# Performance work log

Measured on AMD Instinct MI355X. Metric: run time of the kernel, lower is better.

Reference implementation:

```python
import jax, jax.numpy as jnp
import numpy as np

H = 128  # hidden_size

def _lstm_layer(x, w_ih, w_hh, b_ih, b_hh):
    # x: [B, T, D]; w_ih: [4H, D]; w_hh: [4H, H]; biases: [4H]
    B, T, _ = x.shape
    # Precompute input contributions for all timesteps (the big GEMM).
    xg = jnp.einsum('btd,gd->btg', x, w_ih) + b_ih + b_hh  # [B, T, 4H]
    xg = jnp.transpose(xg, (1, 0, 2))  # [T, B, 4H]
    w_hh_t = w_hh.T  # [H, 4H]

    def step(carry, xt):
        h, c = carry
        g = xt + h @ w_hh_t  # [B, 4H]
        i, f, gg, o = jnp.split(g, 4, axis=-1)  # PyTorch gate order i,f,g,o
        i = jax.nn.sigmoid(i)
        f = jax.nn.sigmoid(f)
        gg = jnp.tanh(gg)
        o = jax.nn.sigmoid(o)
        c = f * c + i * gg
        h = o * jnp.tanh(c)
        return (h, c), h

    h0 = jnp.zeros((B, H), dtype=x.dtype)
    c0 = jnp.zeros((B, H), dtype=x.dtype)
    _, hs = jax.lax.scan(step, (h0, c0), xg)  # hs: [T, B, H]
    return jnp.transpose(hs, (1, 0, 2))  # [B, T, H]

def setup_inputs() -> dict:
    key = jax.random.key(0)
    ks = jax.random.split(key, 11)
    s = 1.0 / np.sqrt(H)  # PyTorch LSTM init scale
    return {
        'x': jax.random.normal(ks[0], (128, 512, 1024), dtype=jnp.float32),
        'w_ih0': jax.random.normal(ks[1], (4 * H, 1024), dtype=jnp.float32) * s,
        'w_hh0': jax.random.normal(ks[2], (4 * H, H), dtype=jnp.float32) * s,
        'b_ih0': jax.random.normal(ks[3], (4 * H,), dtype=jnp.float32) * s,
        'b_hh0': jax.random.normal(ks[4], (4 * H,), dtype=jnp.float32) * s,
        'w_ih1': jax.random.normal(ks[5], (4 * H, H), dtype=jnp.float32) * s,
        'w_hh1': jax.random.normal(ks[6], (4 * H, H), dtype=jnp.float32) * s,
        'b_ih1': jax.random.normal(ks[7], (4 * H,), dtype=jnp.float32) * s,
        'b_hh1': jax.random.normal(ks[8], (4 * H,), dtype=jnp.float32) * s,
        'fc_w': jax.random.normal(ks[9], (8, H), dtype=jnp.float32) * s,
        'fc_b': jax.random.normal(ks[10], (8,), dtype=jnp.float32) * s,
    }

def reference(x, w_ih0, w_hh0, b_ih0, b_hh0, w_ih1, w_hh1, b_ih1, b_hh1, fc_w, fc_b):
    h1 = _lstm_layer(x, w_ih0, w_hh0, b_ih0, b_hh0)   # [B, T, H]
    h2 = _lstm_layer(h1, w_ih1, w_hh1, b_ih1, b_hh1)  # [B, T, H]
    logits = h2[:, -1, :] @ fc_w.T + fc_b             # [B, num_classes]
    return logits
```

## Files before the change

kernel.cpp:

```cpp
#include <hip/hip_runtime.h>
#include <hip/hip_bf16.h>

#define BATCH 128
#define TSTEPS 512
#define HID 128
#define GATES 512
#define M_TOTAL (BATCH * TSTEPS)

typedef _Float16 h2_t __attribute__((ext_vector_type(2)));

__device__ __forceinline__ float sigmoidf_fast(float x) {
    return 1.0f / (1.0f + __expf(-x));
}
__device__ __forceinline__ float tanhf_fast(float x) {
    return 1.0f - 2.0f / (__expf(2.0f * x) + 1.0f);
}

__device__ __forceinline__ float fdot2h(h2_t a, h2_t b, float c) {
#if __has_builtin(__builtin_amdgcn_fdot2)
    return __builtin_amdgcn_fdot2(a, b, c, false);
#else
    return c + (float)a[0] * (float)b[0] + (float)a[1] * (float)b[1];
#endif
}

template<int K>
__global__ __launch_bounds__(256) void gemm_bias_k(
    const float* __restrict__ A,
    const float* __restrict__ W,
    const float* __restrict__ b0,
    const float* __restrict__ b1,
    float* __restrict__ xgT)
{
    constexpr int BM = 128, BN = 128, BK = 16;
    __shared__ float As[BK][BM];
    __shared__ float Bs[BK][BN];

    const int tid = threadIdx.x;
    const int tx = tid & 15;
    const int ty = tid >> 4;
    const int n0 = blockIdx.x * BN;
    const int m0 = blockIdx.y * BM;

    const int f0 = tid, f1 = tid + 256;
    const int ar0 = f0 >> 2, ak0 = (f0 & 3) * 4;
    const int ar1 = f1 >> 2, ak1 = (f1 & 3) * 4;

    const float* pa0 = A + (size_t)(m0 + ar0) * K + ak0;
    const float* pa1 = A + (size_t)(m0 + ar1) * K + ak1;
    const float* pw0 = W + (size_t)(n0 + ar0) * K + ak0;
    const float* pw1 = W + (size_t)(n0 + ar1) * K + ak1;

    float bias8[8];
    #pragma unroll
    for (int j = 0; j < 8; ++j) {
        int n = n0 + ((j < 4) ? (tx * 4 + j) : (64 + tx * 4 + j - 4));
        bias8[j] = b0[n] + b1[n];
    }
    float acc[8][8];
    #pragma unroll
    for (int i = 0; i < 8; ++i)
        #pragma unroll
        for (int j = 0; j < 8; ++j) acc[i][j] = bias8[j];

    for (int k0 = 0; k0 < K; k0 += BK) {
        const float4 a0 = *(const float4*)(pa0 + k0);
        const float4 a1 = *(const float4*)(pa1 + k0);
        const float4 w0 = *(const float4*)(pw0 + k0);
        const float4 w1 = *(const float4*)(pw1 + k0);
        __syncthreads();
        As[ak0 + 0][ar0] = a0.x; As[ak0 + 1][ar0] = a0.y;
        As[ak0 + 2][ar0] = a0.z; As[ak0 + 3][ar0] = a0.w;
        As[ak1 + 0][ar1] = a1.x; As[ak1 + 1][ar1] = a1.y;
        As[ak1 + 2][ar1] = a1.z; As[ak1 + 3][ar1] = a1.w;
        Bs[ak0 + 0][ar0] = w0.x; Bs[ak0 + 1][ar0] = w0.y;
        Bs[ak0 + 2][ar0] = w0.z; Bs[ak0 + 3][ar0] = w0.w;
        Bs[ak1 + 0][ar1] = w1.x; Bs[ak1 + 1][ar1] = w1.y;
        Bs[ak1 + 2][ar1] = w1.z; Bs[ak1 + 3][ar1] = w1.w;
        __syncthreads();
        #pragma unroll
        for (int kk = 0; kk < BK; ++kk) {
            const float4 av0 = *(const float4*)&As[kk][ty * 8];
            const float4 av1 = *(const float4*)&As[kk][ty * 8 + 4];
            const float4 bv0 = *(const float4*)&Bs[kk][tx * 4];
            const float4 bv1 = *(const float4*)&Bs[kk][64 + tx * 4];
            const float a[8]  = {av0.x, av0.y, av0.z, av0.w, av1.x, av1.y, av1.z, av1.w};
            const float bb[8] = {bv0.x, bv0.y, bv0.z, bv0.w, bv1.x, bv1.y, bv1.z, bv1.w};
            #pragma unroll
            for (int i = 0; i < 8; ++i)
                #pragma unroll
                for (int j = 0; j < 8; ++j)
                    acc[i][j] = __fmaf_rn(a[i], bb[j], acc[i][j]);
        }
    }

    const int bi = m0 >> 9;
    const int t0 = (m0 & 511) + ty * 8;
    float4* xo = (float4*)xgT;
    #pragma unroll
    for (int j = 0; j < 8; ++j) {
        const int n = n0 + ((j < 4) ? (tx * 4 + j) : (64 + tx * 4 + j - 4));
        float4 v0 = make_float4(acc[0][j], acc[1][j], acc[2][j], acc[3][j]);
        float4 v1 = make_float4(acc[4][j], acc[5][j], acc[6][j], acc[7][j]);
        xo[(size_t)(bi * 128 + (t0 >> 2)) * 512 + n]     = v0;
        xo[(size_t)(bi * 128 + (t0 >> 2) + 1) * 512 + n] = v1;
    }
}

__global__ __launch_bounds__(1024, 4) void fused_rec(
    const float* __restrict__ xgT,
    const float* __restrict__ w_hh0,
    const float* __restrict__ w_ih1,
    const float* __restrict__ w_hh1,
    const float* __restrict__ b_ih1,
    const float* __restrict__ b_hh1,
    const float* __restrict__ fc_w,
    const float* __restrict__ fc_b,
    unsigned int* __restrict__ h1g,
    int* __restrict__ flags,
    float* __restrict__ logits)
{
    const int blk = blockIdx.x;
    const int L1  = blk >= BATCH;
    const int b   = blk & (BATCH - 1);
    const int tid = threadIdx.x;
    const int g   = tid >> 1;
    const int kh  = tid & 1;

    __shared__ h2_t h2s[64];
    __shared__ float act_s[GATES];
    __shared__ h2_t hin2[8 * 64];

    h2_t whh[32], wih[32];
    {
        const float* wr = (L1 ? w_hh1 : w_hh0) + (size_t)g * HID + kh * 64;
        #pragma unroll
        for (int i = 0; i < 32; ++i)
            whh[i] = (h2_t){(_Float16)wr[2 * i], (_Float16)wr[2 * i + 1]};
    }
    float bias = 0.f;
    if (L1) {
        const float* wr = w_ih1 + (size_t)g * HID + kh * 64;
        #pragma unroll
        for (int i = 0; i < 32; ++i)
            wih[i] = (h2_t){(_Float16)wr[2 * i], (_Float16)wr[2 * i + 1]};
        if (kh == 0) bias = b_ih1[g] + b_hh1[g];
    }

    if (tid < 64) h2s[tid] = (h2_t){(_Float16)0.f, (_Float16)0.f};
    float c = 0.f;

    const float4* xgTb = (const float4*)xgT + (size_t)b * 128 * 512 + g;
    float4 cur4 = make_float4(0.f, 0.f, 0.f, 0.f);
    if (!L1 && kh == 0) cur4 = xgTb[0];

    unsigned int* h1row = h1g + (size_t)b * TSTEPS * 64;
    int* flagb = flags + b * 64;

    __syncthreads();

    float4 xv4 = cur4;
    for (int t8 = 0; t8 < 64; ++t8) {
        if (L1) {
            if (tid < 64) {
                while (__hip_atomic_load(&flagb[tid], __ATOMIC_ACQUIRE,
                                         __HIP_MEMORY_SCOPE_AGENT) < t8 + 1) {}
                #pragma unroll
                for (int r = 0; r < 8; ++r) {
                    union { unsigned int u; h2_t h; } cv;
                    cv.u = h1row[(size_t)(t8 * 8 + r) * 64 + tid];
                    hin2[r * 64 + tid] = cv.h;
                }
            }
            __syncthreads();
        }
        #pragma unroll
        for (int u = 0; u < 8; ++u) {
            const int t = t8 * 8 + u;
            if (u == 0 || u == 4) {
                xv4 = cur4;
                if (!L1 && kh == 0) {
                    int tc = (t >> 2) + 1; if (tc > 127) tc = 127;
                    cur4 = xgTb[(size_t)tc * 512];
                }
            }
            const float xv = ((u & 3) == 0) ? xv4.x : ((u & 3) == 1) ? xv4.y
                           : ((u & 3) == 2) ? xv4.z : xv4.w;

            float p0 = 0.f, p1 = 0.f;
            const h2_t* hb = h2s + kh * 32;
            #pragma unroll
            for (int i = 0; i < 32; i += 2) {
                p0 = fdot2h(whh[i],     hb[i],     p0);
                p1 = fdot2h(whh[i + 1], hb[i + 1], p1);
            }
            if (L1) {
                const h2_t* xb = hin2 + u * 64 + kh * 32;
                #pragma unroll
                for (int i = 0; i < 32; i += 2) {
                    p0 = fdot2h(wih[i],     xb[i],     p0);
                    p1 = fdot2h(wih[i + 1], xb[i + 1], p1);
                }
            }
            float p = p0 + p1;
            p += __shfl_xor(p, 1);
            if (kh == 0) {
                const float s = p + (L1 ? bias : xv);
                act_s[g] = (g >= 256 && g < 384) ? tanhf_fast(s) : sigmoidf_fast(s);
            }
            __syncthreads();
            if (tid < HID) {
                const float ig = act_s[tid];
                const float fg = act_s[tid + 128];
                const float gg = act_s[tid + 256];
                const float og = act_s[tid + 384];
                c = __fmaf_rn(fg, c, ig * gg);
                const float h = og * tanhf_fast(c);
                const float hn = __shfl_down(h, 1);
                if ((tid & 1) == 0) {
                    union { h2_t h; unsigned int u; } pk;
                    pk.h = (h2_t){(_Float16)h, (_Float16)hn};
                    h2s[tid >> 1] = pk.h;
                    if (!L1)
                        __hip_atomic_store(&h1row[(size_t)t * 64 + (tid >> 1)], pk.u,
                                           __ATOMIC_RELAXED, __HIP_MEMORY_SCOPE_AGENT);
                }
                if (L1 && t == TSTEPS - 1) act_s[tid] = h;
            }
            __syncthreads();
        }
        if (!L1 && tid < HID && (tid & 1) == 0)
            __hip_atomic_store(&flagb[tid >> 1], t8 + 1,
                               __ATOMIC_RELEASE, __HIP_MEMORY_SCOPE_AGENT);
    }

    if (L1 && tid < 8) {
        float s = fc_b[tid];
        const float* wr = fc_w + tid * HID;
        #pragma unroll 4
        for (int k = 0; k < HID; ++k) s = __fmaf_rn(wr[k], act_s[k], s);
        logits[b * 8 + tid] = s;
    }
}

extern "C" void kernel_launch(void* const* d_in, const int* in_sizes, int n_in,
                              void* d_out, int out_size, void* d_ws, size_t ws_size,
                              hipStream_t stream) {
    const float* x     = (const float*)d_in[0];
    const float* w_ih0 = (const float*)d_in[1];
    const float* w_hh0 = (const float*)d_in[2];
    const float* b_ih0 = (const float*)d_in[3];
    const float* b_hh0 = (const float*)d_in[4];
    const float* w_ih1 = (const float*)d_in[5];
    const float* w_hh1 = (const float*)d_in[6];
    const float* b_ih1 = (const float*)d_in[7];
    const float* b_hh1 = (const float*)d_in[8];
    const float* fc_w  = (const float*)d_in[9];
    const float* fc_b  = (const float*)d_in[10];
    float* out = (float*)d_out;

    float*        xgT   = (float*)d_ws;
    unsigned int* h1g   = (unsigned int*)((char*)d_ws + (size_t)M_TOTAL * GATES * 4);
    int*          flags = (int*)((char*)d_ws + (size_t)M_TOTAL * GATES * 4
                                             + (size_t)BATCH * TSTEPS * 64 * 4);

    dim3 gg(4, 512);
    gemm_bias_k<1024><<<gg, dim3(256), 0, stream>>>(x, w_ih0, b_ih0, b_hh0, xgT);
    fused_rec<<<dim3(2 * BATCH), dim3(1024), 0, stream>>>(
        xgT, w_hh0, w_ih1, w_hh1, b_ih1, b_hh1, fc_w, fc_b, h1g, flags, out);
}
```

Measured before the change: 1.748 ms.

## Use split-fp16 MFMA GEMM and single-thread-per-gate recurrence with prefetched layer coupling

The input-projection GEMM moves from FP32 FMA to 16x16x32 fp16 MFMA. Both operands are split into hi/lo halves and three MFMAs per tile recover near-fp32 accuracy, with the weights pre-split by a small conversion kernel. The recurrent kernel drops from 1024 to 512 threads, one gate row per thread, which removes the shuffle reduction. Layer 1 now waits on layer 0 every 4 steps and prefetches inputs ahead through a ring buffer instead of blocking every 8 steps. Risks include the extra MFMA work, the rewritten flag protocol between layers, and higher register pressure from 128 packed weights per thread.

```diff
diff --git a/kernel.cpp b/kernel.cpp
--- a/kernel.cpp
+++ b/kernel.cpp
@@ -7,7 +7,10 @@
 #define GATES 512
 #define M_TOTAL (BATCH * TSTEPS)
 
-typedef _Float16 h2_t __attribute__((ext_vector_type(2)));
+typedef _Float16 h2_t  __attribute__((ext_vector_type(2)));
+typedef _Float16 half4 __attribute__((ext_vector_type(4)));
+typedef _Float16 half8 __attribute__((ext_vector_type(8)));
+typedef float    f32x4 __attribute__((ext_vector_type(4)));
 
 __device__ __forceinline__ float sigmoidf_fast(float x) {
     return 1.0f / (1.0f + __expf(-x));
@@ -15,7 +18,6 @@
 __device__ __forceinline__ float tanhf_fast(float x) {
     return 1.0f - 2.0f / (__expf(2.0f * x) + 1.0f);
 }
-
 __device__ __forceinline__ float fdot2h(h2_t a, h2_t b, float c) {
 #if __has_builtin(__builtin_amdgcn_fdot2)
     return __builtin_amdgcn_fdot2(a, b, c, false);
@@ -24,91 +26,133 @@
 #endif
 }
 
-template<int K>
-__global__ __launch_bounds__(256) void gemm_bias_k(
+__global__ __launch_bounds__(256) void convert_w(
+    const float* __restrict__ src, _Float16* __restrict__ hi, _Float16* __restrict__ lo)
+{
+    const int i = blockIdx.x * 256 + threadIdx.x;
+    float4 v = ((const float4*)src)[i];
+    half4 h, l;
+    h[0] = (_Float16)v.x; l[0] = (_Float16)(v.x - (float)h[0]);
+    h[1] = (_Float16)v.y; l[1] = (_Float16)(v.y - (float)h[1]);
+    h[2] = (_Float16)v.z; l[2] = (_Float16)(v.z - (float)h[2]);
+    h[3] = (_Float16)v.w; l[3] = (_Float16)(v.w - (float)h[3]);
+    *(half4*)&hi[4 * i] = h;
+    *(half4*)&lo[4 * i] = l;
+}
+
+__global__ __launch_bounds__(256, 2) void gemm_mfma(
     const float* __restrict__ A,
-    const float* __restrict__ W,
+    const _Float16* __restrict__ Wh,
+    const _Float16* __restrict__ Wl,
     const float* __restrict__ b0,
     const float* __restrict__ b1,
-    float* __restrict__ xgT)
+    float* __restrict__ xg)
 {
-    constexpr int BM = 128, BN = 128, BK = 16;
-    __shared__ float As[BK][BM];
-    __shared__ float Bs[BK][BN];
+    constexpr int K = 1024;
+    __shared__ __align__(16) _Float16 sXh[128 * 32];
+    __shared__ __align__(16) _Float16 sXl[128 * 32];
+    __shared__ __align__(16) _Float16 sWh[128 * 32];
+    __shared__ __align__(16) _Float16 sWl[128 * 32];
 
     const int tid = threadIdx.x;
-    const int tx = tid & 15;
-    const int ty = tid >> 4;
-    const int n0 = blockIdx.x * BN;
-    const int m0 = blockIdx.y * BM;
-
-    const int f0 = tid, f1 = tid + 256;
-    const int ar0 = f0 >> 2, ak0 = (f0 & 3) * 4;
-    const int ar1 = f1 >> 2, ak1 = (f1 & 3) * 4;
-
-    const float* pa0 = A + (size_t)(m0 + ar0) * K + ak0;
-    const float* pa1 = A + (size_t)(m0 + ar1) * K + ak1;
-    const float* pw0 = W + (size_t)(n0 + ar0) * K + ak0;
-    const float* pw1 = W + (size_t)(n0 + ar1) * K + ak1;
-
-    float bias8[8];
+    const int lane = tid & 63, wv = tid >> 6;
+    const int wm = wv & 1, wn = wv >> 1;
+    const int n0 = blockIdx.x * 128;
+    const int m0 = blockIdx.y * 128;
+
+    const int ar = tid & 127, aks = (tid >> 7) * 16;
+    const float* pA = A + (size_t)(m0 + ar) * K + aks;
+    const _Float16* pWh0 = Wh + (size_t)(n0 + (tid & 127)) * K + (tid >> 7) * 8;
+    const _Float16* pWl0 = Wl + (size_t)(n0 + (tid & 127)) * K + (tid >> 7) * 8;
+
+    f32x4 acc[4][4];
     #pragma unroll
-    for (int j = 0; j < 8; ++j) {
-        int n = n0 + ((j < 4) ? (tx * 4 + j) : (64 + tx * 4 + j - 4));
-        bias8[j] = b0[n] + b1[n];
-    }
-    float acc[8][8];
+    for (int nt = 0; nt < 4; ++nt) {
+        const int cn = n0 + wn * 64 + nt * 16 + (lane & 15);
+        const float bv = b0[cn] + b1[cn];
+        #pragma unroll
+        for (int mt = 0; mt < 4; ++mt) acc[mt][nt] = (f32x4){bv, bv, bv, bv};
+    }
+
+    float xv[16];
+    half8 w0h, w1h, w0l, w1l;
     #pragma unroll
-    for (int i = 0; i < 8; ++i)
-        #pragma unroll
-        for (int j = 0; j < 8; ++j) acc[i][j] = bias8[j];
-
-    for (int k0 = 0; k0 < K; k0 += BK) {
-        const float4 a0 = *(const float4*)(pa0 + k0);
-        const float4 a1 = *(const float4*)(pa1 + k0);
-        const float4 w0 = *(const float4*)(pw0 + k0);
-        const float4 w1 = *(const float4*)(pw1 + k0);
+    for (int j = 0; j < 4; ++j) *(float4*)&xv[4 * j] = *(const float4*)(pA + 4 * j);
+    w0h = *(const half8*)(pWh0);      w1h = *(const half8*)(pWh0 + 16);
+    w0l = *(const half8*)(pWl0);      w1l = *(const half8*)(pWl0 + 16);
+
+    const int kb0 = (tid >> 7) * 2;
+    for (int ks = 0; ks < 32; ++ks) {
+        half8 hh0, hh1, hl0, hl1;
+        #pragma unroll
+        for (int j = 0; j < 8; ++j) {
+            _Float16 h = (_Float16)xv[j];
+            hh0[j] = h; hl0[j] = (_Float16)(xv[j] - (float)h);
+        }
+        #pragma unroll
+        for (int j = 0; j < 8; ++j) {
+            _Float16 h = (_Float16)xv[8 + j];
+            hh1[j] = h; hl1[j] = (_Float16)(xv[8 + j] - (float)h);
+        }
+        if (ks) __syncthreads();
+        *(half8*)&sXh[(size_t)((kb0    ) * 128 + ar) * 8] = hh0;
+        *(half8*)&sXh[(size_t)((kb0 + 1) * 128 + ar) * 8] = hh1;
+        *(half8*)&sXl[(size_t)((kb0    ) * 128 + ar) * 8] = hl0;
+        *(half8*)&sXl[(size_t)((kb0 + 1) * 128 + ar) * 8] = hl1;
+        *(half8*)&sWh[(size_t)tid * 8]         = w0h;
+        *(half8*)&sWh[(size_t)(tid + 256) * 8] = w1h;
+        *(half8*)&sWl[(size_t)tid * 8]         = w0l;
+        *(half8*)&sWl[(size_t)(tid + 256) * 8] = w1l;
         __syncthreads();
-        As[ak0 + 0][ar0] = a0.x; As[ak0 + 1][ar0] = a0.y;
-        As[ak0 + 2][ar0] = a0.z; As[ak0 + 3][ar0] = a0.w;
-        As[ak1 + 0][ar1] = a1.x; As[ak1 + 1][ar1] = a1.y;
-        As[ak1 + 2][ar1] = a1.z; As[ak1 + 3][ar1] = a1.w;
-        Bs[ak0 + 0][ar0] = w0.x; Bs[ak0 + 1][ar0] = w0.y;
-        Bs[ak0 + 2][ar0] = w0.z; Bs[ak0 + 3][ar0] = w0.w;
-        Bs[ak1 + 0][ar1] = w1.x; Bs[ak1 + 1][ar1] = w1.y;
-        Bs[ak1 + 2][ar1] = w1.z; Bs[ak1 + 3][ar1] = w1.w;
-        __syncthreads();
-        #pragma unroll
-        for (int kk = 0; kk < BK; ++kk) {
-            const float4 av0 = *(const float4*)&As[kk][ty * 8];
-            const float4 av1 = *(const float4*)&As[kk][ty * 8 + 4];
-            const float4 bv0 = *(const float4*)&Bs[kk][tx * 4];
-            const float4 bv1 = *(const float4*)&Bs[kk][64 + tx * 4];
-            const float a[8]  = {av0.x, av0.y, av0.z, av0.w, av1.x, av1.y, av1.z, av1.w};
-            const float bb[8] = {bv0.x, bv0.y, bv0.z, bv0.w, bv1.x, bv1.y, bv1.z, bv1.w};
+
+        if (ks < 31) {
+            const int kn = (ks + 1) * 32;
             #pragma unroll
-            for (int i = 0; i < 8; ++i)
-                #pragma unroll
-                for (int j = 0; j < 8; ++j)
-                    acc[i][j] = __fmaf_rn(a[i], bb[j], acc[i][j]);
-        }
-    }
-
-    const int bi = m0 >> 9;
-    const int t0 = (m0 & 511) + ty * 8;
-    float4* xo = (float4*)xgT;
+            for (int j = 0; j < 4; ++j)
+                *(float4*)&xv[4 * j] = *(const float4*)(pA + kn + 4 * j);
+            w0h = *(const half8*)(pWh0 + kn);      w1h = *(const half8*)(pWh0 + kn + 16);
+            w0l = *(const half8*)(pWl0 + kn);      w1l = *(const half8*)(pWl0 + kn + 16);
+        }
+
+        const int fr = lane & 15, kb = lane >> 4;
+        half8 ah[4], al[4], bh[4], bl[4];
+        #pragma unroll
+        for (int mt = 0; mt < 4; ++mt) {
+            const int idx = (kb * 128 + wm * 64 + mt * 16 + fr) * 8;
+            ah[mt] = *(const half8*)&sXh[idx];
+            al[mt] = *(const half8*)&sXl[idx];
+        }
+        #pragma unroll
+        for (int nt = 0; nt < 4; ++nt) {
+            const int idx = (kb * 128 + wn * 64 + nt * 16 + fr) * 8;
+            bh[nt] = *(const half8*)&sWh[idx];
+            bl[nt] = *(const half8*)&sWl[idx];
+        }
+        #pragma unroll
+        for (int mt = 0; mt < 4; ++mt)
+            #pragma unroll
+            for (int nt = 0; nt < 4; ++nt) {
+                acc[mt][nt] = __builtin_amdgcn_mfma_f32_16x16x32_f16(ah[mt], bh[nt], acc[mt][nt], 0, 0, 0);
+                acc[mt][nt] = __builtin_amdgcn_mfma_f32_16x16x32_f16(ah[mt], bl[nt], acc[mt][nt], 0, 0, 0);
+                acc[mt][nt] = __builtin_amdgcn_mfma_f32_16x16x32_f16(al[mt], bh[nt], acc[mt][nt], 0, 0, 0);
+            }
+    }
+
     #pragma unroll
-    for (int j = 0; j < 8; ++j) {
-        const int n = n0 + ((j < 4) ? (tx * 4 + j) : (64 + tx * 4 + j - 4));
-        float4 v0 = make_float4(acc[0][j], acc[1][j], acc[2][j], acc[3][j]);
-        float4 v1 = make_float4(acc[4][j], acc[5][j], acc[6][j], acc[7][j]);
-        xo[(size_t)(bi * 128 + (t0 >> 2)) * 512 + n]     = v0;
-        xo[(size_t)(bi * 128 + (t0 >> 2) + 1) * 512 + n] = v1;
-    }
-}
-
-__global__ __launch_bounds__(1024, 4) void fused_rec(
-    const float* __restrict__ xgT,
+    for (int mt = 0; mt < 4; ++mt) {
+        const int rm = m0 + wm * 64 + mt * 16 + (lane >> 4) * 4;
+        #pragma unroll
+        for (int nt = 0; nt < 4; ++nt) {
+            const int cn = n0 + wn * 64 + nt * 16 + (lane & 15);
+            #pragma unroll
+            for (int r = 0; r < 4; ++r)
+                xg[(size_t)(rm + r) * GATES + cn] = acc[mt][nt][r];
+        }
+    }
+}
+
+__global__ __launch_bounds__(512, 2) void fused_rec2(
+    const float* __restrict__ xg,
     const float* __restrict__ w_hh0,
     const float* __restrict__ w_ih1,
     const float* __restrict__ w_hh1,
@@ -121,125 +165,139 @@
     float* __restrict__ logits)
 {
     const int blk = blockIdx.x;
-    const int L1  = blk >= BATCH;
-    const int b   = blk & (BATCH - 1);
-    const int tid = threadIdx.x;
-    const int g   = tid >> 1;
-    const int kh  = tid & 1;
-
-    __shared__ h2_t h2s[64];
-    __shared__ float act_s[GATES];
-    __shared__ h2_t hin2[8 * 64];
-
-    h2_t whh[32], wih[32];
+    const bool L1 = blk >= BATCH;
+    const int b = blk & (BATCH - 1);
+    const int g = threadIdx.x;
+
+    __shared__ __align__(16) _Float16 h16[HID];
+    __shared__ __align__(16) float act_s[GATES];
+    __shared__ __align__(16) unsigned int hin[8][64];
+    __shared__ __align__(16) float hfin[HID];
+
+    h2_t whh[64], wih[64];
     {
-        const float* wr = (L1 ? w_hh1 : w_hh0) + (size_t)g * HID + kh * 64;
-        #pragma unroll
-        for (int i = 0; i < 32; ++i)
-            whh[i] = (h2_t){(_Float16)wr[2 * i], (_Float16)wr[2 * i + 1]};
+        const float4* w4 = (const float4*)((L1 ? w_hh1 : w_hh0) + (size_t)g * HID);
+        #pragma unroll
+        for (int i = 0; i < 32; ++i) {
+            float4 v = w4[i];
+            whh[2 * i]     = (h2_t){(_Float16)v.x, (_Float16)v.y};
+            whh[2 * i + 1] = (h2_t){(_Float16)v.z, (_Float16)v.w};
+        }
     }
     float bias = 0.f;
     if (L1) {
-        const float* wr = w_ih1 + (size_t)g * HID + kh * 64;
-        #pragma unroll
-        for (int i = 0; i < 32; ++i)
-            wih[i] = (h2_t){(_Float16)wr[2 * i], (_Float16)wr[2 * i + 1]};
-        if (kh == 0) bias = b_ih1[g] + b_hh1[g];
-    }
-
-    if (tid < 64) h2s[tid] = (h2_t){(_Float16)0.f, (_Float16)0.f};
+        const float4* w4 = (const float4*)(w_ih1 + (size_t)g * HID);
+        #pragma unroll
+        for (int i = 0; i < 32; ++i) {
+            float4 v = w4[i];
+            wih[2 * i]     = (h2_t){(_Float16)v.x, (_Float16)v.y};
+            wih[2 * i + 1] = (h2_t){(_Float16)v.z, (_Float16)v.w};
+        }
+        bias = b_ih1[g] + b_hh1[g];
+    }
+
+    if (g < HID) h16[g] = (_Float16)0.f;
     float c = 0.f;
-
-    const float4* xgTb = (const float4*)xgT + (size_t)b * 128 * 512 + g;
-    float4 cur4 = make_float4(0.f, 0.f, 0.f, 0.f);
-    if (!L1 && kh == 0) cur4 = xgTb[0];
 
     unsigned int* h1row = h1g + (size_t)b * TSTEPS * 64;
     int* flagb = flags + b * 64;
 
+    if (L1 && g < 64) {
+        while (__hip_atomic_load(&flagb[g], __ATOMIC_ACQUIRE, __HIP_MEMORY_SCOPE_AGENT) < 8) {}
+        #pragma unroll
+        for (int d = 0; d < 8; ++d)
+            hin[d][g] = __hip_atomic_load(&h1row[(size_t)d * 64 + g],
+                                          __ATOMIC_RELAXED, __HIP_MEMORY_SCOPE_AGENT);
+    }
+
+    const float* xgb = xg + (size_t)b * TSTEPS * GATES + g;
+    float xcur[4], xnxt[4];
+    if (!L1) {
+        #pragma unroll
+        for (int u = 0; u < 4; ++u) xcur[u] = xgb[(size_t)u * GATES];
+    }
     __syncthreads();
 
-    float4 xv4 = cur4;
-    for (int t8 = 0; t8 < 64; ++t8) {
-        if (L1) {
-            if (tid < 64) {
-                while (__hip_atomic_load(&flagb[tid], __ATOMIC_ACQUIRE,
-                                         __HIP_MEMORY_SCOPE_AGENT) < t8 + 1) {}
+    for (int t4 = 0; t4 < 128; ++t4) {
+        if (!L1) {
+            const int tn = (t4 + 1 < 128) ? (t4 + 1) * 4 : t4 * 4;
+            #pragma unroll
+            for (int u = 0; u < 4; ++u) xnxt[u] = xgb[(size_t)(tn + u) * GATES];
+        }
+        #pragma unroll
+        for (int u = 0; u < 4; ++u) {
+            const int t = t4 * 4 + u;
+            float p0 = 0.f, p1 = 0.f, p2 = 0.f, p3 = 0.f;
+            {
+                const half8* hv = (const half8*)h16;
                 #pragma unroll
-                for (int r = 0; r < 8; ++r) {
-                    union { unsigned int u; h2_t h; } cv;
-                    cv.u = h1row[(size_t)(t8 * 8 + r) * 64 + tid];
-                    hin2[r * 64 + tid] = cv.h;
+                for (int j = 0; j < 16; ++j) {
+                    half8 hh = hv[j];
+                    p0 = fdot2h(whh[4 * j],     (h2_t){hh[0], hh[1]}, p0);
+                    p1 = fdot2h(whh[4 * j + 1], (h2_t){hh[2], hh[3]}, p1);
+                    p2 = fdot2h(whh[4 * j + 2], (h2_t){hh[4], hh[5]}, p2);
+                    p3 = fdot2h(whh[4 * j + 3], (h2_t){hh[6], hh[7]}, p3);
                 }
             }
+            if (L1) {
+                const half8* xv8 = (const half8*)&hin[t & 7][0];
+                #pragma unroll
+                for (int j = 0; j < 16; ++j) {
+                    half8 hh = xv8[j];
+                    p0 = fdot2h(wih[4 * j],     (h2_t){hh[0], hh[1]}, p0);
+                    p1 = fdot2h(wih[4 * j + 1], (h2_t){hh[2], hh[3]}, p1);
+                    p2 = fdot2h(wih[4 * j + 2], (h2_t){hh[4], hh[5]}, p2);
+                    p3 = fdot2h(wih[4 * j + 3], (h2_t){hh[6], hh[7]}, p3);
+                }
+            }
+            const float s = (p0 + p1) + (p2 + p3) + (L1 ? bias : xcur[u]);
+            act_s[g] = ((g >> 7) == 2) ? tanhf_fast(s) : sigmoidf_fast(s);
             __syncthreads();
-        }
-        #pragma unroll
-        for (int u = 0; u < 8; ++u) {
-            const int t = t8 * 8 + u;
-            if (u == 0 || u == 4) {
-                xv4 = cur4;
-                if (!L1 && kh == 0) {
-                    int tc = (t >> 2) + 1; if (tc > 127) tc = 127;
-                    cur4 = xgTb[(size_t)tc * 512];
-                }
-            }
-            const float xv = ((u & 3) == 0) ? xv4.x : ((u & 3) == 1) ? xv4.y
-                           : ((u & 3) == 2) ? xv4.z : xv4.w;
-
-            float p0 = 0.f, p1 = 0.f;
-            const h2_t* hb = h2s + kh * 32;
-            #pragma unroll
-            for (int i = 0; i < 32; i += 2) {
-                p0 = fdot2h(whh[i],     hb[i],     p0);
-                p1 = fdot2h(whh[i + 1], hb[i + 1], p1);
-            }
-            if (L1) {
-                const h2_t* xb = hin2 + u * 64 + kh * 32;
-                #pragma unroll
-                for (int i = 0; i < 32; i += 2) {
-                    p0 = fdot2h(wih[i],     xb[i],     p0);
-                    p1 = fdot2h(wih[i + 1], xb[i + 1], p1);
-                }
-            }
-            float p = p0 + p1;
-            p += __shfl_xor(p, 1);
-            if (kh == 0) {
-                const float s = p + (L1 ? bias : xv);
-                act_s[g] = (g >= 256 && g < 384) ? tanhf_fast(s) : sigmoidf_fast(s);
-            }
-            __syncthreads();
-            if (tid < HID) {
-                const float ig = act_s[tid];
-                const float fg = act_s[tid + 128];
-                const float gg = act_s[tid + 256];
-                const float og = act_s[tid + 384];
+            if (g < HID) {
+                const float ig = act_s[g];
+                const float fg = act_s[g + 128];
+                const float gg = act_s[g + 256];
+                const float og = act_s[g + 384];
                 c = __fmaf_rn(fg, c, ig * gg);
                 const float h = og * tanhf_fast(c);
-                const float hn = __shfl_down(h, 1);
-                if ((tid & 1) == 0) {
-                    union { h2_t h; unsigned int u; } pk;
-                    pk.h = (h2_t){(_Float16)h, (_Float16)hn};
-                    h2s[tid >> 1] = pk.h;
-                    if (!L1)
-                        __hip_atomic_store(&h1row[(size_t)t * 64 + (tid >> 1)], pk.u,
-                                           __ATOMIC_RELAXED, __HIP_MEMORY_SCOPE_AGENT);
+                h16[g] = (_Float16)h;
+                if (L1 && t == TSTEPS - 1) hfin[g] = h;
+            }
+            __syncthreads();
+            if (!L1 && g < 64) {
+                __hip_atomic_store(&h1row[(size_t)t * 64 + g], ((const unsigned int*)h16)[g],
+                                   __ATOMIC_RELAXED, __HIP_MEMORY_SCOPE_AGENT);
+                if (u == 3)
+                    __hip_atomic_store(&flagb[g], t + 1,
+                                       __ATOMIC_RELEASE, __HIP_MEMORY_SCOPE_AGENT);
+            }
+            if (L1 && g < 64 && u == 3) {
+                const int tgt = t + 5;
+                if (tgt + 3 < TSTEPS) {
+                    while (__hip_atomic_load(&flagb[g], __ATOMIC_ACQUIRE,
+                                             __HIP_MEMORY_SCOPE_AGENT) < tgt + 4) {}
+                    #pragma unroll
+                    for (int d = 0; d < 4; ++d)
+                        hin[(tgt + d) & 7][g] =
+                            __hip_atomic_load(&h1row[(size_t)(tgt + d) * 64 + g],
+                                              __ATOMIC_RELAXED, __HIP_MEMORY_SCOPE_AGENT);
                 }
-                if (L1 && t == TSTEPS - 1) act_s[tid] = h;
-            }
-            __syncthreads();
-        }
-        if (!L1 && tid < HID && (tid & 1) == 0)
-            __hip_atomic_store(&flagb[tid >> 1], t8 + 1,
-                               __ATOMIC_RELEASE, __HIP_MEMORY_SCOPE_AGENT);
-    }
-
-    if (L1 && tid < 8) {
-        float s = fc_b[tid];
-        const float* wr = fc_w + tid * HID;
-        #pragma unroll 4
-        for (int k = 0; k < HID; ++k) s = __fmaf_rn(wr[k], act_s[k], s);
-        logits[b * 8 + tid] = s;
+            }
+        }
+        if (!L1) {
+            xcur[0] = xnxt[0]; xcur[1] = xnxt[1]; xcur[2] = xnxt[2]; xcur[3] = xnxt[3];
+        }
+    }
+
+    if (L1) {
+        __syncthreads();
+        if (g < 8) {
+            float s2 = fc_b[g];
+            const float* wr = fc_w + g * HID;
+            #pragma unroll 4
+            for (int k2 = 0; k2 < HID; ++k2) s2 = __fmaf_rn(wr[k2], hfin[k2], s2);
+            logits[b * 8 + g] = s2;
+        }
     }
 }
 
@@ -259,13 +317,16 @@
     const float* fc_b  = (const float*)d_in[10];
     float* out = (float*)d_out;
 
-    float*        xgT   = (float*)d_ws;
-    unsigned int* h1g   = (unsigned int*)((char*)d_ws + (size_t)M_TOTAL * GATES * 4);
-    int*          flags = (int*)((char*)d_ws + (size_t)M_TOTAL * GATES * 4
-                                             + (size_t)BATCH * TSTEPS * 64 * 4);
-
-    dim3 gg(4, 512);
-    gemm_bias_k<1024><<<gg, dim3(256), 0, stream>>>(x, w_ih0, b_ih0, b_hh0, xgT);
-    fused_rec<<<dim3(2 * BATCH), dim3(1024), 0, stream>>>(
-        xgT, w_hh0, w_ih1, w_hh1, b_ih1, b_hh1, fc_w, fc_b, h1g, flags, out);
-}
+    char* ws = (char*)d_ws;
+    float*        xgb   = (float*)ws;
+    _Float16*     Whp   = (_Float16*)(ws + (size_t)M_TOTAL * GATES * 4);
+    _Float16*     Wlp   = (_Float16*)(ws + (size_t)M_TOTAL * GATES * 4 + 1048576);
+    unsigned int* h1g   = (unsigned int*)(ws + (size_t)M_TOTAL * GATES * 4 + 2097152);
+    int*          flags = (int*)(ws + (size_t)M_TOTAL * GATES * 4 + 2097152
+                                    + (size_t)BATCH * TSTEPS * 64 * 4);
+
+    convert_w<<<dim3(512), dim3(256), 0, stream>>>(w_ih0, Whp, Wlp);
+    gemm_mfma<<<dim3(4, 512), dim3(256), 0, stream>>>(x, Whp, Wlp, b_ih0, b_hh0, xgb);
+    fused_rec2<<<dim3(2 * BATCH), dim3(512), 0, stream>>>(
+        xgb, w_hh0, w_ih1, w_hh1, b_ih1, b_hh1, fc_w, fc_b, h1g, flags, out);
+}
```

Measured after the change: 1.501 ms. 14.1% less time.
